# Kernel tuning notes

Measured on AMD Instinct MI355X. Metric: run time of the kernel, lower is better.

Reference implementation:

```python
import jax, jax.numpy as jnp
import numpy as np

D_MODEL = 768
N_HEADS = 4
HEAD_DIM = D_MODEL // N_HEADS


def setup_inputs() -> dict:
    key = jax.random.key(0)
    ks = jax.random.split(key, 9)
    B, S = 4, 2048
    scale = 1.0 / np.sqrt(D_MODEL)
    inputs = jax.random.normal(ks[0], (B, S, D_MODEL), dtype=jnp.float32)
    # Linear weights stored as [in, out] for x @ W + b
    Wq = jax.random.normal(ks[1], (D_MODEL, D_MODEL), dtype=jnp.float32) * scale
    bq = jnp.zeros((D_MODEL,), dtype=jnp.float32)
    Wk = jax.random.normal(ks[2], (D_MODEL, D_MODEL), dtype=jnp.float32) * scale
    bk = jnp.zeros((D_MODEL,), dtype=jnp.float32)
    Wv = jax.random.normal(ks[3], (D_MODEL, D_MODEL), dtype=jnp.float32) * scale
    bv = jnp.zeros((D_MODEL,), dtype=jnp.float32)
    Wo = jax.random.normal(ks[4], (D_MODEL, D_MODEL), dtype=jnp.float32) * scale
    bo = jnp.zeros((D_MODEL,), dtype=jnp.float32)
    return {"inputs": inputs, "Wq": Wq, "bq": bq, "Wk": Wk, "bk": bk,
            "Wv": Wv, "bv": bv, "Wo": Wo, "bo": bo}


def reference(inputs, Wq, bq, Wk, bk, Wv, bv, Wo, bo):
    B, S, _ = inputs.shape
    H, Dh = N_HEADS, HEAD_DIM
    # projections -> [B, H, S, Dh]
    def split_heads(x):
        return x.reshape(B, S, H, Dh).transpose(0, 2, 1, 3)
    Q = split_heads(inputs @ Wq + bq)
    K = split_heads(inputs @ Wk + bk)
    V = split_heads(inputs @ Wv + bv)
    scores = jnp.einsum('bhqd,bhkd->bhqk', Q, K) / jnp.sqrt(jnp.float32(Dh))
    causal = jnp.tril(jnp.ones((S, S), dtype=bool))  # True = keep
    scores = jnp.where(causal, scores, -jnp.inf)
    weights = jax.nn.softmax(scores, axis=-1)
    # dropout is identity in eval mode
    ctx = jnp.einsum('bhqk,bhkd->bhqd', weights, V)
    ctx = ctx.transpose(0, 2, 1, 3).reshape(B, S, H * Dh)
    return ctx @ Wo + bo
```

## Files before the change

kernel.cpp:

```cpp
#include <hip/hip_runtime.h>
#include <hip/hip_bf16.h>
#include <cstddef>

typedef __attribute__((ext_vector_type(8))) short short8;
typedef __attribute__((ext_vector_type(4))) float f32x4;
typedef __attribute__((ext_vector_type(16))) float f32x16;
typedef __attribute__((ext_vector_type(4))) unsigned short u16x4;

#define D_MODEL 768
#define N_HEADS 4
#define HEAD_DIM 192
#define BATCH 4
#define SEQ 2048
#define M_ROWS (BATCH*SEQ)

__device__ __forceinline__ short f2bf(float f) {
  union { float f; unsigned u; } v; v.f = f;
  unsigned r = v.u + 0x7FFFu + ((v.u >> 16) & 1u);
  return (short)(r >> 16);
}

__device__ __forceinline__ float fexp2(float x) {
  return __builtin_amdgcn_exp2f(x);
}

__device__ __forceinline__ void gl_lds16(const void* g, void* l) {
  __builtin_amdgcn_global_load_lds(
      (const __attribute__((address_space(1))) void*)g,
      (__attribute__((address_space(3))) void*)l, 16, 0, 0);
}

__global__ __launch_bounds__(256) void cast_kernel(const float* __restrict__ src,
                                                   short* __restrict__ dst, int n8) {
  int i = blockIdx.x * 256 + threadIdx.x;
  if (i >= n8) return;
  const float4* s = (const float4*)src;
  float4 a = s[2 * i], b = s[2 * i + 1];
  short8 o;
  o[0] = f2bf(a.x); o[1] = f2bf(a.y); o[2] = f2bf(a.z); o[3] = f2bf(a.w);
  o[4] = f2bf(b.x); o[5] = f2bf(b.y); o[6] = f2bf(b.z); o[7] = f2bf(b.w);
  *(short8*)(dst + (size_t)i * 8) = o;
}

__global__ __launch_bounds__(256) void wtrans(const float* __restrict__ W,
                                              short* __restrict__ Wt) {
  __shared__ float tile[32][33];
  int k0 = blockIdx.x * 32, n0 = blockIdx.y * 32;
  int tc = threadIdx.x & 31, tr = threadIdx.x >> 5;
#pragma unroll
  for (int i = 0; i < 4; i++)
    tile[tr + i * 8][tc] = W[(size_t)(k0 + tr + i * 8) * D_MODEL + n0 + tc];
  __syncthreads();
#pragma unroll
  for (int i = 0; i < 4; i++)
    Wt[(size_t)(n0 + tr + i * 8) * D_MODEL + k0 + tc] = f2bf(tile[tc][tr + i * 8]);
}

__global__ __launch_bounds__(256) void bias_concat(const float* __restrict__ a,
                                                   const float* __restrict__ b,
                                                   const float* __restrict__ c,
                                                   float* __restrict__ dst) {
  int i = blockIdx.x * 256 + threadIdx.x;
  if (i >= 3 * D_MODEL) return;
  float v = i < 768 ? a[i] : (i < 1536 ? b[i - 768] : c[i - 1536]);
  dst[i] = v;
}

template <int MODE>
__global__ __launch_bounds__(256, 4) void gemm_bf16(const short* __restrict__ A,
                                                    const short* __restrict__ Wt,
                                                    const float* __restrict__ bias,
                                                    short* __restrict__ oQ,
                                                    short* __restrict__ oK,
                                                    short* __restrict__ oV,
                                                    float* __restrict__ oF, int N) {
  __shared__ short As[128 * 64];
  __shared__ short Bs[128 * 64];
  const int K = 768;
  const int m0 = blockIdx.x * 128, n0 = blockIdx.y * 128;
  const int t = threadIdx.x, lane = t & 63, w = t >> 6;
  const int wr = w >> 1, wc = w & 1, lr = lane & 15, lg = lane >> 4;

  f32x4 acc[4][4] = {};

  for (int k0 = 0; k0 < K; k0 += 64) {
#pragma unroll
    for (int i = 0; i < 4; i++) {
      int id = w * 4 + i;
      int row = id * 8 + (lane >> 3);
      int cc = (lane & 7) ^ (row & 7);
      gl_lds16(A + (size_t)(m0 + row) * K + k0 + cc * 8, As + id * 512);
      gl_lds16(Wt + (size_t)(n0 + row) * K + k0 + cc * 8, Bs + id * 512);
    }
    __syncthreads();
#pragma unroll
    for (int kb = 0; kb < 2; kb++) {
      short8 a[4], b[4];
#pragma unroll
      for (int m = 0; m < 4; m++) {
        int row = wr * 64 + m * 16 + lr;
        a[m] = *(const short8*)&As[row * 64 + (((kb * 4 + lg) ^ (row & 7)) << 3)];
      }
#pragma unroll
      for (int n = 0; n < 4; n++) {
        int row = wc * 64 + n * 16 + lr;
        b[n] = *(const short8*)&Bs[row * 64 + (((kb * 4 + lg) ^ (row & 7)) << 3)];
      }
#pragma unroll
      for (int m = 0; m < 4; m++)
#pragma unroll
        for (int n = 0; n < 4; n++)
          acc[m][n] = __builtin_amdgcn_mfma_f32_16x16x32_bf16(a[m], b[n], acc[m][n], 0, 0, 0);
    }
    __syncthreads();
  }

  if (MODE == 0) {
#pragma unroll
    for (int m = 0; m < 4; m++)
#pragma unroll
      for (int n = 0; n < 4; n++) {
        int col = n0 + wc * 64 + n * 16 + lr;
        float bv = bias[col];
#pragma unroll
        for (int r = 0; r < 4; r++) {
          int row = m0 + wr * 64 + m * 16 + lg * 4 + r;
          oF[(size_t)row * N + col] = acc[m][n][r] + bv;
        }
      }
  } else {
    const int bb = m0 >> 11;
#pragma unroll
    for (int m = 0; m < 4; m++) {
      int s0 = (m0 & (SEQ - 1)) + wr * 64 + m * 16 + lg * 4;
#pragma unroll
      for (int n = 0; n < 4; n++) {
        int col = n0 + wc * 64 + n * 16 + lr;
        int seg = col / 768;
        int d = col - seg * 768;
        int h = d / HEAD_DIM, dd = d - h * HEAD_DIM;
        int bh = bb * N_HEADS + h;
        float bv = bias[col];
        if (seg < 2) {
          short* dst = seg == 0 ? oQ : oK;
#pragma unroll
          for (int r = 0; r < 4; r++)
            dst[((size_t)bh * SEQ + s0 + r) * HEAD_DIM + dd] = f2bf(acc[m][n][r] + bv);
        } else {
          u16x4 pk;
#pragma unroll
          for (int r = 0; r < 4; r++) pk[r] = (unsigned short)f2bf(acc[m][n][r] + bv);
          *(u16x4*)&oV[((size_t)bh * HEAD_DIM + dd) * SEQ + s0] = pk;
        }
      }
    }
  }
}

__device__ __forceinline__ void stage_kv(const short* Kp, const short* Vp, int kbase,
                                         short* KsB, short* VsB, int w, int lane) {
#pragma unroll
  for (int i = 0; i < 6; i++) {
    int id = w * 6 + i;
    int o16 = id * 64 + lane;
    int row = o16 / 24, cc0 = o16 - row * 24;
    int cc = cc0 ^ (row & 7);
    gl_lds16(Kp + (size_t)(kbase + row) * HEAD_DIM + cc * 8, KsB + id * 512);
  }
#pragma unroll
  for (int i = 0; i < 6; i++) {
    int id = w * 6 + i;
    int o16 = id * 64 + lane;
    int row = o16 >> 3, cc = (o16 & 7) ^ (row & 7);
    gl_lds16(Vp + (size_t)row * SEQ + kbase + cc * 8, VsB + id * 512);
  }
}

__global__ __launch_bounds__(256, 1) void attn_kernel(const short* __restrict__ Q,
                                                      const short* __restrict__ Kg,
                                                      const short* __restrict__ Vt,
                                                      short* __restrict__ ctx) {
  __shared__ short Ks[2][64 * 192];
  __shared__ short Vs[2][192 * 64];
  float* obuf = (float*)&Vs[0][0];
  float* mlbuf = (float*)&Ks[0][0];

  const int n = blockIdx.x;
  const int slot = n >> 3;
  const int bh = (n & 7) * 2 + (slot >> 4);
  const int p = slot & 15;
  const int b = bh >> 2, head = bh & 3;
  const short* Qp = Q + (size_t)bh * SEQ * HEAD_DIM;
  const short* Kp = Kg + (size_t)bh * SEQ * HEAD_DIM;
  const short* Vp = Vt + (size_t)bh * HEAD_DIM * SEQ;
  const int t = threadIdx.x, lane = t & 63, w = t >> 6;
  const int wq = w >> 1, wk = w & 1;
  const int l31 = lane & 31, hl = lane >> 5;
  const float scale2 = 0.07216878364870322f * 1.4426950408889634f;

  for (int pass = 0; pass < 2; pass++) {
    const int qt = pass ? 31 - p : p;
    const int nkb = qt + 1;
    const int q0w = qt * 64 + wq * 32;
    const int qlane = q0w + l31;

    stage_kv(Kp, Vp, 0, Ks[0], Vs[0], w, lane);

    short8 qf[12];
#pragma unroll
    for (int c = 0; c < 12; c++)
      qf[c] = *(const short8*)&Qp[(size_t)qlane * HEAD_DIM + c * 16 + hl * 8];

    f32x16 oacc[6];
#pragma unroll
    for (int d = 0; d < 6; d++) oacc[d] = 0.f;
    float m = -3.0e38f, lsum = 0.f;

    for (int kb = 0; kb < nkb; kb++) {
      const int cur = kb & 1;
      const int kbase = kb * 64;
      if (kb + 1 < nkb) {
        stage_kv(Kp, Vp, kbase + 64, Ks[cur ^ 1], Vs[cur ^ 1], w, lane);
        asm volatile("s_waitcnt vmcnt(12)" ::: "memory");
      } else {
        asm volatile("s_waitcnt vmcnt(0)" ::: "memory");
      }
      __builtin_amdgcn_s_barrier();
      asm volatile("" ::: "memory");

      if (kbase + wk * 32 <= q0w + 31) {
        const short* KcB = Ks[cur];
        const short* VcB = Vs[cur];

        f32x16 sacc = 0.f;
        const int krow = wk * 32 + l31;
        const int krb = krow * 192;
        const int kswz = (krow & 7) << 3;
#pragma unroll
        for (int c = 0; c < 12; c++) {
          short8 kf = *(const short8*)&KcB[krb + ((c * 16 + hl * 8) ^ kswz)];
          sacc = __builtin_amdgcn_mfma_f32_32x32x16_bf16(kf, qf[c], sacc, 0, 0, 0);
        }

        float s[16];
        const bool need_mask = (kbase + wk * 32 + 31) > q0w;
        const int kb0 = kbase + wk * 32 + 4 * hl;
#pragma unroll
        for (int r = 0; r < 16; r++) {
          float v = sacc[r] * scale2;
          if (need_mask) {
            int kg = kb0 + (r & 3) + 8 * (r >> 2);
            if (kg > qlane) v = -3.0e38f;
          }
          s[r] = v;
        }
        float mx = s[0];
#pragma unroll
        for (int r = 1; r < 16; r++) mx = fmaxf(mx, s[r]);
        mx = fmaxf(mx, __shfl_xor(mx, 32, 64));
        if (!__all(mx <= m + 8.0f)) {
          float mn = fmaxf(m, mx);
          float al = fexp2(m - mn);
          m = mn;
          lsum *= al;
#pragma unroll
          for (int d = 0; d < 6; d++) oacc[d] *= al;
        }
        float pr[16];
        float rs = 0.f;
#pragma unroll
        for (int r = 0; r < 16; r++) {
          pr[r] = fexp2(s[r] - m);
          rs += pr[r];
        }
        rs += __shfl_xor(rs, 32, 64);
        lsum += rs;

        unsigned pk[8], ex[8];
#pragma unroll
        for (int j = 0; j < 8; j++) {
          unsigned r0;
          asm("v_cvt_pk_bf16_f32 %0, %1, %2" : "=v"(r0) : "v"(pr[2 * j]), "v"(pr[2 * j + 1]));
          pk[j] = r0;
        }
#pragma unroll
        for (int j = 0; j < 8; j++) ex[j] = __shfl_xor((int)pk[j], 32, 64);
        union { unsigned u[4]; short8 s8; } f0, f1;
        f0.u[0] = hl ? ex[2] : pk[0];
        f0.u[1] = hl ? ex[3] : pk[1];
        f0.u[2] = hl ? pk[2] : ex[0];
        f0.u[3] = hl ? pk[3] : ex[1];
        f1.u[0] = hl ? ex[6] : pk[4];
        f1.u[1] = hl ? ex[7] : pk[5];
        f1.u[2] = hl ? pk[6] : ex[4];
        f1.u[3] = hl ? pk[7] : ex[5];

#pragma unroll
        for (int db = 0; db < 6; db++) {
          const int vrow = db * 32 + l31;
          const int vrb = vrow * 64;
          const int vswz = (vrow & 7) << 3;
          short8 va = *(const short8*)&VcB[vrb + ((wk * 32 + hl * 8) ^ vswz)];
          oacc[db] = __builtin_amdgcn_mfma_f32_32x32x16_bf16(va, f0.s8, oacc[db], 0, 0, 0);
          short8 vb = *(const short8*)&VcB[vrb + ((wk * 32 + 16 + hl * 8) ^ vswz)];
          oacc[db] = __builtin_amdgcn_mfma_f32_32x32x16_bf16(vb, f1.s8, oacc[db], 0, 0, 0);
        }
      }
      asm volatile("" ::: "memory");
      __builtin_amdgcn_s_barrier();
    }

    __syncthreads();
    if (wk == 1) {
      if (lane < 32) {
        mlbuf[wq * 64 + lane] = m;
        mlbuf[wq * 64 + 32 + lane] = lsum;
      }
#pragma unroll
      for (int db = 0; db < 6; db++)
#pragma unroll
        for (int g = 0; g < 4; g++) {
          int d = db * 32 + 8 * g + 4 * hl;
          f32x4 vv;
          vv[0] = oacc[db][4 * g];
          vv[1] = oacc[db][4 * g + 1];
          vv[2] = oacc[db][4 * g + 2];
          vv[3] = oacc[db][4 * g + 3];
          *(f32x4*)&obuf[(wq * 32 + l31) * 192 + (d ^ ((l31 & 7) << 2))] = vv;
        }
    }
    __syncthreads();
    if (wk == 0) {
      float m1 = mlbuf[wq * 64 + l31];
      float l1 = mlbuf[wq * 64 + 32 + l31];
      float ms = fmaxf(m, m1);
      float a0 = fexp2(m - ms), a1 = fexp2(m1 - ms);
      float lt = lsum * a0 + l1 * a1;
      float rl = 1.0f / lt;
#pragma unroll
      for (int db = 0; db < 6; db++)
#pragma unroll
        for (int g = 0; g < 4; g++) {
          int d = db * 32 + 8 * g + 4 * hl;
          f32x4 rd = *(const f32x4*)&obuf[(wq * 32 + l31) * 192 + (d ^ ((l31 & 7) << 2))];
          u16x4 pkk;
#pragma unroll
          for (int r2 = 0; r2 < 4; r2++) {
            float v = (oacc[db][4 * g + r2] * a0 + rd[r2] * a1) * rl;
            pkk[r2] = (unsigned short)f2bf(v);
          }
          *(u16x4*)&ctx[((size_t)b * SEQ + qlane) * D_MODEL + head * HEAD_DIM + d] = pkk;
        }
    }
    __syncthreads();
  }
}

extern "C" void kernel_launch(void* const* d_in, const int* in_sizes, int n_in,
                              void* d_out, int out_size, void* d_ws, size_t ws_size,
                              hipStream_t stream) {
  const float* X  = (const float*)d_in[0];
  const float* Wq = (const float*)d_in[1];
  const float* bq = (const float*)d_in[2];
  const float* Wk = (const float*)d_in[3];
  const float* bk = (const float*)d_in[4];
  const float* Wv = (const float*)d_in[5];
  const float* bv = (const float*)d_in[6];
  const float* Wo = (const float*)d_in[7];
  const float* bo = (const float*)d_in[8];

  char* ws = (char*)d_ws;
  const size_t XB = (size_t)M_ROWS * D_MODEL * 2;
  const size_t WQKV = (size_t)3 * D_MODEL * D_MODEL * 2;
  const size_t WB = (size_t)D_MODEL * D_MODEL * 2;

  short* Xb    = (short*)(ws);
  short* Wqkvt = (short*)(ws + XB);
  short* Wot   = (short*)(ws + XB + WQKV);
  float* bqkv  = (float*)(ws + XB + WQKV + WB);
  short* Qb    = (short*)(ws + XB + WQKV + WB + 12288);
  short* Kb    = (short*)(ws + XB + WQKV + WB + 12288 + XB);
  short* Vtb   = (short*)(ws + XB + WQKV + WB + 12288 + 2 * XB);
  short* Cb    = (short*)(ws + XB + WQKV + WB + 12288 + 3 * XB);

  const int n8x = M_ROWS * D_MODEL / 8;
  cast_kernel<<<(n8x + 255) / 256, 256, 0, stream>>>(X, Xb, n8x);
  dim3 tg(24, 24);
  wtrans<<<tg, 256, 0, stream>>>(Wq, Wqkvt);
  wtrans<<<tg, 256, 0, stream>>>(Wk, Wqkvt + (size_t)768 * 768);
  wtrans<<<tg, 256, 0, stream>>>(Wv, Wqkvt + (size_t)2 * 768 * 768);
  wtrans<<<tg, 256, 0, stream>>>(Wo, Wot);
  bias_concat<<<9, 256, 0, stream>>>(bq, bk, bv, bqkv);

  gemm_bf16<1><<<dim3(M_ROWS / 128, 2304 / 128), 256, 0, stream>>>(
      Xb, Wqkvt, bqkv, Qb, Kb, Vtb, nullptr, 2304);

  attn_kernel<<<256, 256, 0, stream>>>(Qb, Kb, Vtb, Cb);

  gemm_bf16<0><<<dim3(M_ROWS / 128, 768 / 128), 256, 0, stream>>>(
      Cb, Wot, bo, nullptr, nullptr, nullptr, (float*)d_out, 768);
}
```

Baseline: 154.4 us.

## Single-buffer attention LDS for two blocks per CU, one tile per block

The attention kernel drops K/V double-buffering so LDS per block halves, raises launch bounds to two blocks per CU, and launches 512 blocks that each handle one query tile, with the longest tiles scheduled first instead of pairing tiles inside a block. Each key block now loads synchronously and waits for vmcnt(0), relying on the co-resident block to hide the latency. s_setprio is raised around the MFMA loops. The risks are that the tighter register bound at 2 waves per SIMD causes spills, and that the exposed load latency within each block is not fully hidden by the other block.

```diff
diff --git a/kernel.cpp b/kernel.cpp
--- a/kernel.cpp
+++ b/kernel.cpp
@@ -176,19 +176,21 @@
   }
 }
 
-__global__ __launch_bounds__(256, 1) void attn_kernel(const short* __restrict__ Q,
+__global__ __launch_bounds__(256, 2) void attn_kernel(const short* __restrict__ Q,
                                                       const short* __restrict__ Kg,
                                                       const short* __restrict__ Vt,
                                                       short* __restrict__ ctx) {
-  __shared__ short Ks[2][64 * 192];
-  __shared__ short Vs[2][192 * 64];
-  float* obuf = (float*)&Vs[0][0];
-  float* mlbuf = (float*)&Ks[0][0];
-
-  const int n = blockIdx.x;
-  const int slot = n >> 3;
-  const int bh = (n & 7) * 2 + (slot >> 4);
-  const int p = slot & 15;
+  __shared__ short smem[64 * 192 + 192 * 64];
+  __shared__ float mlbuf[128];
+  short* Ks = smem;
+  short* Vs = smem + 64 * 192;
+  float* obuf = (float*)smem;
+
+  const int i = blockIdx.x;
+  int bh, qt;
+  if (i < 256) { bh = i & 15; qt = 31 - (i >> 4); }
+  else         { int j = i - 256; bh = j & 15; qt = j >> 4; }
+
   const int b = bh >> 2, head = bh & 3;
   const short* Qp = Q + (size_t)bh * SEQ * HEAD_DIM;
   const short* Kp = Kg + (size_t)bh * SEQ * HEAD_DIM;
@@ -198,161 +200,151 @@
   const int l31 = lane & 31, hl = lane >> 5;
   const float scale2 = 0.07216878364870322f * 1.4426950408889634f;
 
-  for (int pass = 0; pass < 2; pass++) {
-    const int qt = pass ? 31 - p : p;
-    const int nkb = qt + 1;
-    const int q0w = qt * 64 + wq * 32;
-    const int qlane = q0w + l31;
-
-    stage_kv(Kp, Vp, 0, Ks[0], Vs[0], w, lane);
-
-    short8 qf[12];
-#pragma unroll
-    for (int c = 0; c < 12; c++)
-      qf[c] = *(const short8*)&Qp[(size_t)qlane * HEAD_DIM + c * 16 + hl * 8];
-
-    f32x16 oacc[6];
-#pragma unroll
-    for (int d = 0; d < 6; d++) oacc[d] = 0.f;
-    float m = -3.0e38f, lsum = 0.f;
-
-    for (int kb = 0; kb < nkb; kb++) {
-      const int cur = kb & 1;
-      const int kbase = kb * 64;
-      if (kb + 1 < nkb) {
-        stage_kv(Kp, Vp, kbase + 64, Ks[cur ^ 1], Vs[cur ^ 1], w, lane);
-        asm volatile("s_waitcnt vmcnt(12)" ::: "memory");
-      } else {
-        asm volatile("s_waitcnt vmcnt(0)" ::: "memory");
-      }
-      __builtin_amdgcn_s_barrier();
-      asm volatile("" ::: "memory");
-
-      if (kbase + wk * 32 <= q0w + 31) {
-        const short* KcB = Ks[cur];
-        const short* VcB = Vs[cur];
-
-        f32x16 sacc = 0.f;
-        const int krow = wk * 32 + l31;
-        const int krb = krow * 192;
-        const int kswz = (krow & 7) << 3;
-#pragma unroll
-        for (int c = 0; c < 12; c++) {
-          short8 kf = *(const short8*)&KcB[krb + ((c * 16 + hl * 8) ^ kswz)];
-          sacc = __builtin_amdgcn_mfma_f32_32x32x16_bf16(kf, qf[c], sacc, 0, 0, 0);
+  const int nkb = qt + 1;
+  const int q0w = qt * 64 + wq * 32;
+  const int qlane = q0w + l31;
+
+  short8 qf[12];
+#pragma unroll
+  for (int c = 0; c < 12; c++)
+    qf[c] = *(const short8*)&Qp[(size_t)qlane * HEAD_DIM + c * 16 + hl * 8];
+
+  f32x16 oacc[6];
+#pragma unroll
+  for (int d = 0; d < 6; d++) oacc[d] = 0.f;
+  float m = -3.0e38f, lsum = 0.f;
+
+  for (int kb = 0; kb < nkb; kb++) {
+    const int kbase = kb * 64;
+    stage_kv(Kp, Vp, kbase, Ks, Vs, w, lane);
+    asm volatile("s_waitcnt vmcnt(0)" ::: "memory");
+    __builtin_amdgcn_s_barrier();
+    asm volatile("" ::: "memory");
+
+    if (kbase + wk * 32 <= q0w + 31) {
+      f32x16 sacc = 0.f;
+      const int krow = wk * 32 + l31;
+      const int krb = krow * 192;
+      const int kswz = (krow & 7) << 3;
+      __builtin_amdgcn_s_setprio(1);
+#pragma unroll
+      for (int c = 0; c < 12; c++) {
+        short8 kf = *(const short8*)&Ks[krb + ((c * 16 + hl * 8) ^ kswz)];
+        sacc = __builtin_amdgcn_mfma_f32_32x32x16_bf16(kf, qf[c], sacc, 0, 0, 0);
+      }
+      __builtin_amdgcn_s_setprio(0);
+
+      float s[16];
+      const bool need_mask = (kbase + wk * 32 + 31) > q0w;
+      const int kb0 = kbase + wk * 32 + 4 * hl;
+#pragma unroll
+      for (int r = 0; r < 16; r++) {
+        float v = sacc[r] * scale2;
+        if (need_mask) {
+          int kg = kb0 + (r & 3) + 8 * (r >> 2);
+          if (kg > qlane) v = -3.0e38f;
         }
-
-        float s[16];
-        const bool need_mask = (kbase + wk * 32 + 31) > q0w;
-        const int kb0 = kbase + wk * 32 + 4 * hl;
-#pragma unroll
-        for (int r = 0; r < 16; r++) {
-          float v = sacc[r] * scale2;
-          if (need_mask) {
-            int kg = kb0 + (r & 3) + 8 * (r >> 2);
-            if (kg > qlane) v = -3.0e38f;
-          }
-          s[r] = v;
+        s[r] = v;
+      }
+      float mx = s[0];
+#pragma unroll
+      for (int r = 1; r < 16; r++) mx = fmaxf(mx, s[r]);
+      mx = fmaxf(mx, __shfl_xor(mx, 32, 64));
+      if (!__all(mx <= m + 8.0f)) {
+        float mn = fmaxf(m, mx);
+        float al = fexp2(m - mn);
+        m = mn;
+        lsum *= al;
+#pragma unroll
+        for (int d = 0; d < 6; d++) oacc[d] *= al;
+      }
+      float pr[16];
+      float rs = 0.f;
+#pragma unroll
+      for (int r = 0; r < 16; r++) {
+        pr[r] = fexp2(s[r] - m);
+        rs += pr[r];
+      }
+      rs += __shfl_xor(rs, 32, 64);
+      lsum += rs;
+
+      unsigned pk[8], ex[8];
+#pragma unroll
+      for (int j = 0; j < 8; j++) {
+        unsigned r0;
+        asm("v_cvt_pk_bf16_f32 %0, %1, %2" : "=v"(r0) : "v"(pr[2 * j]), "v"(pr[2 * j + 1]));
+        pk[j] = r0;
+      }
+#pragma unroll
+      for (int j = 0; j < 8; j++) ex[j] = __shfl_xor((int)pk[j], 32, 64);
+      union { unsigned u[4]; short8 s8; } f0, f1;
+      f0.u[0] = hl ? ex[2] : pk[0];
+      f0.u[1] = hl ? ex[3] : pk[1];
+      f0.u[2] = hl ? pk[2] : ex[0];
+      f0.u[3] = hl ? pk[3] : ex[1];
+      f1.u[0] = hl ? ex[6] : pk[4];
+      f1.u[1] = hl ? ex[7] : pk[5];
+      f1.u[2] = hl ? pk[6] : ex[4];
+      f1.u[3] = hl ? pk[7] : ex[5];
+
+      __builtin_amdgcn_s_setprio(1);
+#pragma unroll
+      for (int db = 0; db < 6; db++) {
+        const int vrow = db * 32 + l31;
+        const int vrb = vrow * 64;
+        const int vswz = (vrow & 7) << 3;
+        short8 va = *(const short8*)&Vs[vrb + ((wk * 32 + hl * 8) ^ vswz)];
+        oacc[db] = __builtin_amdgcn_mfma_f32_32x32x16_bf16(va, f0.s8, oacc[db], 0, 0, 0);
+        short8 vb = *(const short8*)&Vs[vrb + ((wk * 32 + 16 + hl * 8) ^ vswz)];
+        oacc[db] = __builtin_amdgcn_mfma_f32_32x32x16_bf16(vb, f1.s8, oacc[db], 0, 0, 0);
+      }
+      __builtin_amdgcn_s_setprio(0);
+    }
+    asm volatile("" ::: "memory");
+    __builtin_amdgcn_s_barrier();
+  }
+
+  __syncthreads();
+  if (wk == 1) {
+    if (lane < 32) {
+      mlbuf[wq * 64 + lane] = m;
+      mlbuf[wq * 64 + 32 + lane] = lsum;
+    }
+#pragma unroll
+    for (int db = 0; db < 6; db++)
+#pragma unroll
+      for (int g = 0; g < 4; g++) {
+        int d = db * 32 + 8 * g + 4 * hl;
+        f32x4 vv;
+        vv[0] = oacc[db][4 * g];
+        vv[1] = oacc[db][4 * g + 1];
+        vv[2] = oacc[db][4 * g + 2];
+        vv[3] = oacc[db][4 * g + 3];
+        *(f32x4*)&obuf[(wq * 32 + l31) * 192 + (d ^ ((l31 & 7) << 2))] = vv;
+      }
+  }
+  __syncthreads();
+  if (wk == 0) {
+    float m1 = mlbuf[wq * 64 + l31];
+    float l1 = mlbuf[wq * 64 + 32 + l31];
+    float ms = fmaxf(m, m1);
+    float a0 = fexp2(m - ms), a1 = fexp2(m1 - ms);
+    float lt = lsum * a0 + l1 * a1;
+    float rl = 1.0f / lt;
+#pragma unroll
+    for (int db = 0; db < 6; db++)
+#pragma unroll
+      for (int g = 0; g < 4; g++) {
+        int d = db * 32 + 8 * g + 4 * hl;
+        f32x4 rd = *(const f32x4*)&obuf[(wq * 32 + l31) * 192 + (d ^ ((l31 & 7) << 2))];
+        u16x4 pkk;
+#pragma unroll
+        for (int r2 = 0; r2 < 4; r2++) {
+          float v = (oacc[db][4 * g + r2] * a0 + rd[r2] * a1) * rl;
+          pkk[r2] = (unsigned short)f2bf(v);
         }
-        float mx = s[0];
-#pragma unroll
-        for (int r = 1; r < 16; r++) mx = fmaxf(mx, s[r]);
-        mx = fmaxf(mx, __shfl_xor(mx, 32, 64));
-        if (!__all(mx <= m + 8.0f)) {
-          float mn = fmaxf(m, mx);
-          float al = fexp2(m - mn);
-          m = mn;
-          lsum *= al;
-#pragma unroll
-          for (int d = 0; d < 6; d++) oacc[d] *= al;
-        }
-        float pr[16];
-        float rs = 0.f;
-#pragma unroll
-        for (int r = 0; r < 16; r++) {
-          pr[r] = fexp2(s[r] - m);
-          rs += pr[r];
-        }
-        rs += __shfl_xor(rs, 32, 64);
-        lsum += rs;
-
-        unsigned pk[8], ex[8];
-#pragma unroll
-        for (int j = 0; j < 8; j++) {
-          unsigned r0;
-          asm("v_cvt_pk_bf16_f32 %0, %1, %2" : "=v"(r0) : "v"(pr[2 * j]), "v"(pr[2 * j + 1]));
-          pk[j] = r0;
-        }
-#pragma unroll
-        for (int j = 0; j < 8; j++) ex[j] = __shfl_xor((int)pk[j], 32, 64);
-        union { unsigned u[4]; short8 s8; } f0, f1;
-        f0.u[0] = hl ? ex[2] : pk[0];
-        f0.u[1] = hl ? ex[3] : pk[1];
-        f0.u[2] = hl ? pk[2] : ex[0];
-        f0.u[3] = hl ? pk[3] : ex[1];
-        f1.u[0] = hl ? ex[6] : pk[4];
-        f1.u[1] = hl ? ex[7] : pk[5];
-        f1.u[2] = hl ? pk[6] : ex[4];
-        f1.u[3] = hl ? pk[7] : ex[5];
-
-#pragma unroll
-        for (int db = 0; db < 6; db++) {
-          const int vrow = db * 32 + l31;
-          const int vrb = vrow * 64;
-          const int vswz = (vrow & 7) << 3;
-          short8 va = *(const short8*)&VcB[vrb + ((wk * 32 + hl * 8) ^ vswz)];
-          oacc[db] = __builtin_amdgcn_mfma_f32_32x32x16_bf16(va, f0.s8, oacc[db], 0, 0, 0);
-          short8 vb = *(const short8*)&VcB[vrb + ((wk * 32 + 16 + hl * 8) ^ vswz)];
-          oacc[db] = __builtin_amdgcn_mfma_f32_32x32x16_bf16(vb, f1.s8, oacc[db], 0, 0, 0);
-        }
-      }
-      asm volatile("" ::: "memory");
-      __builtin_amdgcn_s_barrier();
-    }
-
-    __syncthreads();
-    if (wk == 1) {
-      if (lane < 32) {
-        mlbuf[wq * 64 + lane] = m;
-        mlbuf[wq * 64 + 32 + lane] = lsum;
-      }
-#pragma unroll
-      for (int db = 0; db < 6; db++)
-#pragma unroll
-        for (int g = 0; g < 4; g++) {
-          int d = db * 32 + 8 * g + 4 * hl;
-          f32x4 vv;
-          vv[0] = oacc[db][4 * g];
-          vv[1] = oacc[db][4 * g + 1];
-          vv[2] = oacc[db][4 * g + 2];
-          vv[3] = oacc[db][4 * g + 3];
-          *(f32x4*)&obuf[(wq * 32 + l31) * 192 + (d ^ ((l31 & 7) << 2))] = vv;
-        }
-    }
-    __syncthreads();
-    if (wk == 0) {
-      float m1 = mlbuf[wq * 64 + l31];
-      float l1 = mlbuf[wq * 64 + 32 + l31];
-      float ms = fmaxf(m, m1);
-      float a0 = fexp2(m - ms), a1 = fexp2(m1 - ms);
-      float lt = lsum * a0 + l1 * a1;
-      float rl = 1.0f / lt;
-#pragma unroll
-      for (int db = 0; db < 6; db++)
-#pragma unroll
-        for (int g = 0; g < 4; g++) {
-          int d = db * 32 + 8 * g + 4 * hl;
-          f32x4 rd = *(const f32x4*)&obuf[(wq * 32 + l31) * 192 + (d ^ ((l31 & 7) << 2))];
-          u16x4 pkk;
-#pragma unroll
-          for (int r2 = 0; r2 < 4; r2++) {
-            float v = (oacc[db][4 * g + r2] * a0 + rd[r2] * a1) * rl;
-            pkk[r2] = (unsigned short)f2bf(v);
-          }
-          *(u16x4*)&ctx[((size_t)b * SEQ + qlane) * D_MODEL + head * HEAD_DIM + d] = pkk;
-        }
-    }
-    __syncthreads();
+        *(u16x4*)&ctx[((size_t)b * SEQ + qlane) * D_MODEL + head * HEAD_DIM + d] = pkk;
+      }
   }
 }
 
@@ -395,7 +387,7 @@
   gemm_bf16<1><<<dim3(M_ROWS / 128, 2304 / 128), 256, 0, stream>>>(
       Xb, Wqkvt, bqkv, Qb, Kb, Vtb, nullptr, 2304);
 
-  attn_kernel<<<256, 256, 0, stream>>>(Qb, Kb, Vtb, Cb);
+  attn_kernel<<<512, 256, 0, stream>>>(Qb, Kb, Vtb, Cb);
 
   gemm_bf16<0><<<dim3(M_ROWS / 128, 768 / 128), 256, 0, stream>>>(
       Cb, Wot, bo, nullptr, nullptr, nullptr, (float*)d_out, 768);
```

New measurement: 144.7 us. 1.07x faster.
